# Performance work log

Measured on AMD Instinct MI355X. Metric: run time of the kernel, lower is better.

Reference implementation:

```python
import jax, jax.numpy as jnp
import numpy as np
from jax import lax

EPS = 1e-4  # BatchNorm eps from the module

def maxpool2x2(x):
    # x: [N, C, H, W] -> 2x2 max pool, stride 2, no padding
    return lax.reduce_window(x, -jnp.inf, lax.max, (1, 1, 2, 2), (1, 1, 2, 2), 'VALID')

def conv_nchw(x, w):
    return lax.conv_general_dilated(x, w, window_strides=(1, 1), padding='VALID',
                                    dimension_numbers=('NCHW', 'OIHW', 'NCHW'))

def setup_inputs() -> dict:
    key = jax.random.key(0)
    ks = jax.random.split(key, 6)
    return {
        'x':       jax.random.normal(ks[0], (8192, 1, 32, 32), dtype=jnp.float32),
        'conv1_w': jax.random.normal(ks[1], (20, 1, 5, 5), dtype=jnp.float32) * 0.1,
        'conv2_w': jax.random.normal(ks[2], (50, 20, 5, 5), dtype=jnp.float32) * 0.1,
        'lin_w':   jax.random.normal(ks[3], (500, 1250), dtype=jnp.float32) * 0.05,
        'fc_w':    jax.random.normal(ks[4], (10, 500), dtype=jnp.float32) * 0.05,
        'fc_b':    jax.random.normal(ks[5], (10,), dtype=jnp.float32) * 0.05,
    }

def reference(x, conv1_w, conv2_w, lin_w, fc_w, fc_b):
    # --- features ---
    # Conv2d(1, 20, k=5, bias=False): [N,1,32,32] -> [N,20,28,28]
    h = conv_nchw(x, conv1_w)
    # BatchNorm2d(20, eps=1e-4, affine=False), training-mode batch stats (biased var)
    mean = jnp.mean(h, axis=(0, 2, 3), keepdims=True)
    var = jnp.var(h, axis=(0, 2, 3), keepdims=True)
    h = (h - mean) * lax.rsqrt(var + EPS)
    # ReLU + MaxPool 2x2: -> [N,20,14,14]
    h = maxpool2x2(jnp.maximum(h, 0.0))
    # Binarize(): sign of activations
    h = jnp.sign(h)
    # Conv2dBinary(20, 50, k=5): XNOR-style conv = conv with sign(W), scaled by
    # per-output-channel alpha = mean(|W|). -> [N,50,10,10]
    alpha2 = jnp.mean(jnp.abs(conv2_w), axis=(1, 2, 3)).reshape(1, -1, 1, 1)
    h = conv_nchw(h, jnp.sign(conv2_w)) * alpha2
    # Hardtanh + MaxPool 2x2: -> [N,50,5,5]
    h = maxpool2x2(jnp.clip(h, -1.0, 1.0))
    # --- dense ---
    h = h.reshape(h.shape[0], -1)  # [N, 1250], channel-major like torch.flatten
    h = jnp.sign(h)
    # LinearBinary(1250, 500): y = x @ sign(W)^T * alpha, alpha = mean(|W|, dim=1)
    alpha_l = jnp.mean(jnp.abs(lin_w), axis=1)  # [500]
    h = (h @ jnp.sign(lin_w).T) * alpha_l
    h = jnp.clip(h, -1.0, 1.0)
    # fc: Linear(500, num_classes)
    return h @ fc_w.T + fc_b
```

## Files before the change

kernel.cpp:

```cpp
#include <hip/hip_runtime.h>
#include <stdint.h>


#define NIMG 8192

typedef __attribute__((ext_vector_type(8))) _Float16 f16x8;
typedef __attribute__((ext_vector_type(16))) float f32x16;


__global__ __launch_bounds__(256) void prepsum_k(const float* __restrict__ lw,
                                                 const float* __restrict__ w2,
                                                 const float* __restrict__ x,
                                                 unsigned long long* __restrict__ lwp,
                                                 float* __restrict__ alpha,
                                                 uint32_t* __restrict__ wp2,
                                                 float* __restrict__ partial) {
  int b = blockIdx.x, tid = threadIdx.x;
  if (b < 125) {
    int wave = tid >> 6, lane = tid & 63;
    int j = b * 4 + wave;
    float pa = 0.f;
    for (int k = lane; k < 1250; k += 64) pa += fabsf(lw[j * 1250 + k]);
    for (int o = 32; o > 0; o >>= 1) pa += __shfl_down(pa, o, 64);
    if (lane == 0) alpha[j] = pa / 1250.0f;
    if (lane < 20) {
      unsigned long long m = 0;
      int base = j * 1250 + lane * 64;
      int lim = 1250 - lane * 64; if (lim > 64) lim = 64;
      for (int bb = 0; bb < lim; ++bb)
        if (lw[base + bb] > 0.f) m |= (1ull << bb);
      lwp[j * 20 + lane] = m;
    }
  } else if (b < 130) {
    int idx = (b - 125) * 256 + tid;
    if (idx < 1250) {
      int oc = idx / 25, k = idx % 25;
      uint32_t m = 0;
      for (int ic = 0; ic < 20; ++ic)
        if (w2[(oc * 20 + ic) * 25 + k] > 0.f) m |= (1u << ic);
      wp2[idx] = m;
    }
  } else {
    int sb = b - 130;
    const float4* xv = (const float4*)x + (size_t)sb * 16 * 256;
    float ax = 0.f, ay = 0.f, az = 0.f, aw = 0.f;
    for (int nn = 0; nn < 16; ++nn) {
      float4 v = xv[nn * 256 + tid];
      ax += v.x; ay += v.y; az += v.z; aw += v.w;
    }
    float4 r; r.x = ax; r.y = ay; r.z = az; r.w = aw;
    ((float4*)(partial + (size_t)sb * 1024))[tid] = r;
  }
}

__global__ __launch_bounds__(256) void reduce_k(const float* __restrict__ partial,
                                                float* __restrict__ partial2) {
  int b = blockIdx.x, tid = threadIdx.x;
  int e = (b & 3) * 256 + tid;
  int p0 = (b >> 2) * 32;
  float s = 0.f;
#pragma unroll
  for (int p = 0; p < 32; ++p) s += partial[(size_t)(p0 + p) * 1024 + e];
  partial2[(size_t)(b >> 2) * 1024 + e] = s;
}

__global__ __launch_bounds__(256) void mean_k(const float* __restrict__ partial2,
                                              const float* __restrict__ w1,
                                              float* __restrict__ mean) {
  __shared__ float Tsh[1024];
  __shared__ double U8[25][8];
  __shared__ double U[25];
  int t = threadIdx.x;
  for (int e = t; e < 1024; e += 256) {
    double s = 0.0;
#pragma unroll
    for (int b = 0; b < 16; ++b) s += (double)partial2[b * 1024 + e];
    Tsh[e] = (float)s;
  }
  __syncthreads();
  if (t < 200) {
    int tap = t >> 3, part = t & 7;
    int ky = tap / 5, kx = tap % 5;
    double s = 0.0;
    for (int p = part * 98; p < part * 98 + 98; ++p) {
      int py = p / 28, px = p % 28;
      s += (double)Tsh[(py + ky) * 32 + px + kx];
    }
    U8[tap][part] = s;
  }
  __syncthreads();
  if (t < 25) {
    double s = 0.0;
    for (int i = 0; i < 8; ++i) s += U8[t][i];
    U[t] = s;
  }
  __syncthreads();
  if (t < 20) {
    double s = 0.0;
    for (int q = 0; q < 25; ++q) s += (double)w1[t * 25 + q] * U[q];
    mean[t] = (float)(s / (8192.0 * 784.0));
  }
}

__device__ inline uint32_t pack_f16_pair(float fv) {
  _Float16 h = (_Float16)fv;
  float rem = fv - (float)h;
  _Float16 l = (_Float16)(rem * 4096.0f);
  uint32_t hb = (uint32_t)__builtin_bit_cast(unsigned short, h);
  uint32_t lb = (uint32_t)__builtin_bit_cast(unsigned short, l);
  return (hb << 16) | lb;
}

__global__ __launch_bounds__(256, 6) void conv1_mfma_k(const float* __restrict__ x,
                                                       const float* __restrict__ w1,
                                                       const float* __restrict__ mean,
                                                       uint32_t* __restrict__ b1p) {
  __shared__ uint32_t ximg[2][1032];
  int tid = threadIdx.x;
  int wave = tid >> 6, lane = tid & 63;
  int img = wave >> 1, half = wave & 1;
  int n = blockIdx.x * 2 + img;
  uint32_t* xs = ximg[img];

  const float4* xin = (const float4*)(x + (size_t)n * 1024);
#pragma unroll
  for (int i = 0; i < 2; ++i) {
    int idx = (half * 2 + i) * 64 + lane;
    float4 v = xin[idx];
    float fv[4] = {v.x, v.y, v.z, v.w};
#pragma unroll
    for (int e = 0; e < 4; ++e)
      xs[4 * idx + e] = pack_f16_pair(fv[e]);
  }
  if (half == 0 && lane < 8) xs[1024 + lane] = 0;

  int bc = lane & 31;
  int khsel = lane >> 5;
  f16x8 Bh[2], Bhs[2], Bl[2];
  const int t1tab[8] = {8, 9, 18, 19, 20, 21, 22, 23};
  const _Float16 SC = (_Float16)4096.0f;
#pragma unroll
  for (int j = 0; j < 8; ++j) {
    int t0 = j + khsel * 10;
    float wv0 = (bc < 20) ? w1[bc * 25 + t0] : 0.f;
    uint32_t p0 = pack_f16_pair(wv0);
    _Float16 h0 = __builtin_bit_cast(_Float16, (unsigned short)(p0 >> 16));
    Bh[0][j] = h0;
    Bhs[0][j] = h0 * SC;
    Bl[0][j] = __builtin_bit_cast(_Float16, (unsigned short)(p0 & 0xffffu));
    float wv1 = 0.f;
    if (bc < 20) {
      if (khsel == 0) wv1 = w1[bc * 25 + t1tab[j]];
      else if (j == 4) wv1 = w1[bc * 25 + 24];
    }
    uint32_t p1 = pack_f16_pair(wv1);
    _Float16 h1 = __builtin_bit_cast(_Float16, (unsigned short)(p1 >> 16));
    Bh[1][j] = h1;
    Bhs[1][j] = h1 * SC;
    Bl[1][j] = __builtin_bit_cast(_Float16, (unsigned short)(p1 & 0xffffu));
  }
  float mv = (bc < 20) ? mean[bc] * 4096.0f : 3.0e38f;

  int m = lane & 31;
  int d0 = m + khsel * 64;
  int d1 = m + khsel * 4;

  __syncthreads();

  int pp0 = half * 7;
  for (int pp = pp0; pp < pp0 + 7; ++pp) {
    unsigned long long bacc[16];
#pragma unroll
    for (int r = 0; r < 16; ++r) bacc[r] = 0ull;
#pragma unroll
    for (int py2 = 0; py2 < 2; ++py2) {
      int pybase = (2 * pp + py2) * 32;
      const uint32_t* b0 = xs + pybase + d0;
      const uint32_t* b1 = xs + pybase + d1;
      uint32_t raw[16];
      raw[0] = b0[0];   raw[1] = b0[1];   raw[2] = b0[2];   raw[3] = b0[3];
      raw[4] = b0[4];   raw[5] = b0[32];  raw[6] = b0[33];  raw[7] = b0[34];
      raw[8] = b1[35];  raw[9] = b1[36];  raw[10] = b1[99]; raw[11] = b1[100];
      raw[12] = b1[128]; raw[13] = b1[129]; raw[14] = b1[130]; raw[15] = b1[131];
      f16x8 Ah[2], Al[2];
#pragma unroll
      for (int kh = 0; kh < 2; ++kh) {
        uint32_t hw[4], lw2[4];
#pragma unroll
        for (int jj = 0; jj < 4; ++jj) {
          uint32_t v0 = raw[kh * 8 + 2 * jj], v1 = raw[kh * 8 + 2 * jj + 1];
          hw[jj] = __builtin_amdgcn_perm(v1, v0, 0x07060302u);
          lw2[jj] = __builtin_amdgcn_perm(v1, v0, 0x05040100u);
        }
        struct U4 { uint32_t a, b, c, d; };
        U4 hv4 = {hw[0], hw[1], hw[2], hw[3]};
        U4 lv4 = {lw2[0], lw2[1], lw2[2], lw2[3]};
        Ah[kh] = __builtin_bit_cast(f16x8, hv4);
        Al[kh] = __builtin_bit_cast(f16x8, lv4);
      }
      f32x16 acc;
#pragma unroll
      for (int i = 0; i < 16; ++i) acc[i] = 0.f;
      acc = __builtin_amdgcn_mfma_f32_32x32x16_f16(Ah[0], Bhs[0], acc, 0, 0, 0);
      acc = __builtin_amdgcn_mfma_f32_32x32x16_f16(Ah[1], Bhs[1], acc, 0, 0, 0);
      acc = __builtin_amdgcn_mfma_f32_32x32x16_f16(Ah[0], Bl[0], acc, 0, 0, 0);
      acc = __builtin_amdgcn_mfma_f32_32x32x16_f16(Ah[1], Bl[1], acc, 0, 0, 0);
      acc = __builtin_amdgcn_mfma_f32_32x32x16_f16(Al[0], Bh[0], acc, 0, 0, 0);
      acc = __builtin_amdgcn_mfma_f32_32x32x16_f16(Al[1], Bh[1], acc, 0, 0, 0);
#pragma unroll
      for (int r = 0; r < 16; ++r)
        bacc[r] |= __ballot(acc[r] > mv);
    }
    uint32_t pm = 0;
#pragma unroll
    for (int pc = 0; pc < 14; ++pc) {
      int px0 = 2 * pc;
      int r0 = (px0 & 3) + 4 * (px0 >> 3);
      int h0 = (px0 >> 2) & 1;
      unsigned long long mm = bacc[r0] | bacc[r0 + 1];
      uint32_t val = (uint32_t)(mm >> (32 * h0));
      if (lane == pc) pm = val;
    }
    if (lane < 14) b1p[(size_t)n * 196 + pp * 14 + lane] = pm;
  }
}

__global__ __launch_bounds__(512) void conv2lin_k(const uint32_t* __restrict__ b1p,
                                                  const uint32_t* __restrict__ wp2,
                                                  const unsigned long long* __restrict__ lwp,
                                                  const float* __restrict__ alpha,
                                                  const float* __restrict__ fcw,
                                                  const float* __restrict__ fcb,
                                                  float* __restrict__ out) {
  __shared__ uint32_t wsh[1250];
  __shared__ uint32_t bm[8][196];
  __shared__ int sumpc[8][100];
  __shared__ char uni[8][2048];
  int tid = threadIdx.x;
  int wave = tid >> 6, lane = tid & 63;
  int n = blockIdx.x * 8 + wave;
  signed char* s2w = (signed char*)uni[wave];
  float* hshw = (float*)uni[wave];

  for (int i = tid; i < 1250; i += 512) wsh[i] = wp2[i];
#pragma unroll
  for (int rd = 0; rd < 4; ++rd) {
    int idx = rd * 64 + lane;
    if (idx < 196) bm[wave][idx] = b1p[(size_t)n * 196 + idx];
  }
  __syncthreads();

#pragma unroll
  for (int rd = 0; rd < 2; ++rd) {
    int pp = rd * 64 + lane;
    if (pp < 100) {
      int Y = pp / 10, X = pp % 10, s = 0;
#pragma unroll
      for (int ky = 0; ky < 5; ++ky)
#pragma unroll
        for (int kx = 0; kx < 5; ++kx)
          s += __popc(bm[wave][(Y + ky) * 14 + X + kx]);
      sumpc[wave][pp] = s;
    }
  }

#pragma unroll
  for (int rd = 0; rd < 4; ++rd) {
    int unit = rd * 64 + lane;
    if (unit < 250) {
      int oc = unit / 5, r = unit % 5;
      uint32_t w[25];
#pragma unroll
      for (int i = 0; i < 25; ++i) w[i] = wsh[oc * 25 + i];
      for (int pc = 0; pc < 5; ++pc) {
        uint32_t pa[6][6];
#pragma unroll
        for (int rr = 0; rr < 6; ++rr)
#pragma unroll
          for (int cc = 0; cc < 6; ++cc)
            pa[rr][cc] = bm[wave][(2 * r + rr) * 14 + 2 * pc + cc];
        int best = -1000000;
#pragma unroll
        for (int dy = 0; dy < 2; ++dy)
#pragma unroll
          for (int dx = 0; dx < 2; ++dx) {
            int a = 0;
#pragma unroll
            for (int ky = 0; ky < 5; ++ky)
#pragma unroll
              for (int kx = 0; kx < 5; ++kx)
                a += __popc(w[ky * 5 + kx] & pa[dy + ky][dx + kx]);
            a = 2 * a - sumpc[wave][(2 * r + dy) * 10 + 2 * pc + dx];
            if (a > best) best = a;
          }
        s2w[5 * unit + pc] = (signed char)((best > 0) - (best < 0));
      }
    }
  }
  if (lane < 30) s2w[1250 + lane] = 0;

  unsigned long long Pm[20], Nm[20];
  int cp = 0, cn = 0;
#pragma unroll
  for (int k = 0; k < 20; ++k) {
    signed char v = s2w[k * 64 + lane];
    unsigned long long P = __ballot(v > 0);
    unsigned long long N = __ballot(v < 0);
    Pm[k] = P; Nm[k] = N;
    cp += __popcll(P); cn += __popcll(N);
  }

#pragma unroll
  for (int rd = 0; rd < 8; ++rd) {
    int j = rd * 64 + lane;
    float y = 0.f;
    if (j < 500) {
      const ulonglong2* W2 = (const ulonglong2*)(lwp + (size_t)j * 20);
      int a = 0, b = 0;
#pragma unroll
      for (int i = 0; i < 10; ++i) {
        ulonglong2 w2v = W2[i];
        a += __popcll(w2v.x & Pm[2 * i]) + __popcll(w2v.y & Pm[2 * i + 1]);
        b += __popcll(w2v.x & Nm[2 * i]) + __popcll(w2v.y & Nm[2 * i + 1]);
      }
      int dot = 2 * (a - b) - cp + cn;
      y = alpha[j] * (float)dot;
      y = fminf(1.0f, fmaxf(-1.0f, y));
    }
    hshw[rd * 64 + lane] = y;
  }

  float hv[8];
#pragma unroll
  for (int k = 0; k < 8; ++k) hv[k] = hshw[k * 64 + lane];
#pragma unroll
  for (int o = 0; o < 10; ++o) {
    float pa = 0.f;
#pragma unroll
    for (int k = 0; k < 8; ++k) {
      int j = k * 64 + lane;
      if (j < 500) pa += hv[k] * fcw[o * 500 + j];
    }
    for (int off = 32; off > 0; off >>= 1) pa += __shfl_down(pa, off, 64);
    if (lane == 0) out[(size_t)n * 10 + o] = pa + fcb[o];
  }
}

extern "C" void kernel_launch(void* const* d_in, const int* in_sizes, int n_in,
                              void* d_out, int out_size, void* d_ws, size_t ws_size,
                              hipStream_t stream) {
  const float* x   = (const float*)d_in[0];
  const float* w1  = (const float*)d_in[1];
  const float* w2  = (const float*)d_in[2];
  const float* lw  = (const float*)d_in[3];
  const float* fcw = (const float*)d_in[4];
  const float* fcb = (const float*)d_in[5];
  float* out = (float*)d_out;
  char* ws = (char*)d_ws;

  float*    mean  = (float*)(ws + 0);
  uint32_t* wp2   = (uint32_t*)(ws + 128);
  float*    alpha = (float*)(ws + 5632);
  unsigned long long* lwp = (unsigned long long*)(ws + 7680);
  float*    partial = (float*)(ws + 87808);
  uint32_t* b1p   = (uint32_t*)(ws + 2184960);
  float*    partial2 = (float*)(ws + 8607488);

  prepsum_k<<<642, 256, 0, stream>>>(lw, w2, x, lwp, alpha, wp2, partial);
  reduce_k<<<64, 256, 0, stream>>>(partial, partial2);
  mean_k<<<1, 256, 0, stream>>>(partial2, w1, mean);
  conv1_mfma_k<<<4096, 256, 0, stream>>>(x, w1, mean, b1p);
  conv2lin_k<<<1024, 512, 0, stream>>>(b1p, wp2, lwp, alpha, fcw, fcb, out);
}
```

Baseline: 236.9 us.

## Replace popcount binary conv2 with int8 MFMA on unpacked sign planes

The binary conv2 used to run as per-lane AND/popcount loops over packed channel masks. It now runs as int8 32x32x32 MFMA. Activations are expanded in shared memory into 0/1 byte planes per pixel, and weights are pre-packed into ±1 int8 fragments in the prep kernel. The output rows are arranged so that each group of four accumulator entries maps to one 2x2 pool window, which lets the max-pool and sign be applied directly from registers. The cost is a larger shared-memory footprint (about 50KB for planes) and extra prep blocks, and it assumes the MFMA register layouts are correct.

```diff
diff --git a/kernel.cpp b/kernel.cpp
--- a/kernel.cpp
+++ b/kernel.cpp
@@ -6,6 +6,8 @@
 
 typedef __attribute__((ext_vector_type(8))) _Float16 f16x8;
 typedef __attribute__((ext_vector_type(16))) float f32x16;
+typedef __attribute__((ext_vector_type(4))) int i32x4;
+typedef __attribute__((ext_vector_type(16))) int i32x16;
 
 
 __global__ __launch_bounds__(256) void prepsum_k(const float* __restrict__ lw,
@@ -13,7 +15,7 @@
                                                  const float* __restrict__ x,
                                                  unsigned long long* __restrict__ lwp,
                                                  float* __restrict__ alpha,
-                                                 uint32_t* __restrict__ wp2,
+                                                 i32x4* __restrict__ bg,
                                                  float* __restrict__ partial) {
   int b = blockIdx.x, tid = threadIdx.x;
   if (b < 125) {
@@ -31,17 +33,33 @@
         if (lw[base + bb] > 0.f) m |= (1ull << bb);
       lwp[j * 20 + lane] = m;
     }
-  } else if (b < 130) {
+  } else if (b < 138) {
     int idx = (b - 125) * 256 + tid;
-    if (idx < 1250) {
-      int oc = idx / 25, k = idx % 25;
-      uint32_t m = 0;
-      for (int ic = 0; ic < 20; ++ic)
-        if (w2[(oc * 20 + ic) * 25 + k] > 0.f) m |= (1u << ic);
-      wp2[idx] = m;
+    if (idx < 3200) {
+      int t = idx >> 7;
+      int rem = idx & 127;
+      int l = rem & 63;
+      int nt = rem >> 6;
+      int oc = nt * 32 + (l & 31);
+      int hi = l >> 5;
+      i32x4 o4;
+#pragma unroll
+      for (int wi = 0; wi < 4; ++wi) {
+        int word = 0;
+#pragma unroll
+        for (int bb = 0; bb < 4; ++bb) {
+          int k = hi * 16 + wi * 4 + bb;
+          int v = 0;
+          if (k < 20 && oc < 50)
+            v = (w2[(oc * 20 + k) * 25 + t] > 0.f) ? 1 : -1;
+          word |= (v & 0xff) << (8 * bb);
+        }
+        o4[wi] = word;
+      }
+      bg[idx] = o4;
     }
   } else {
-    int sb = b - 130;
+    int sb = b - 138;
     const float4* xv = (const float4*)x + (size_t)sb * 16 * 256;
     float ax = 0.f, ay = 0.f, az = 0.f, aw = 0.f;
     for (int nn = 0; nn < 16; ++nn) {
@@ -225,78 +243,91 @@
   }
 }
 
-__global__ __launch_bounds__(512) void conv2lin_k(const uint32_t* __restrict__ b1p,
-                                                  const uint32_t* __restrict__ wp2,
-                                                  const unsigned long long* __restrict__ lwp,
-                                                  const float* __restrict__ alpha,
-                                                  const float* __restrict__ fcw,
-                                                  const float* __restrict__ fcb,
-                                                  float* __restrict__ out) {
-  __shared__ uint32_t wsh[1250];
-  __shared__ uint32_t bm[8][196];
-  __shared__ int sumpc[8][100];
-  __shared__ char uni[8][2048];
+__global__ __launch_bounds__(512, 4) void conv2lin_k(const uint32_t* __restrict__ b1p,
+                                                     const i32x4* __restrict__ bg,
+                                                     const unsigned long long* __restrict__ lwp,
+                                                     const float* __restrict__ alpha,
+                                                     const float* __restrict__ fcw,
+                                                     const float* __restrict__ fcb,
+                                                     float* __restrict__ out) {
+  __shared__ __attribute__((aligned(16))) char planes[8 * 196 * 32];
+  __shared__ __attribute__((aligned(16))) char uni[8][2048];
   int tid = threadIdx.x;
   int wave = tid >> 6, lane = tid & 63;
-  int n = blockIdx.x * 8 + wave;
+  int n0 = blockIdx.x * 8;
+
+#pragma unroll
+  for (int r = 0; r < 4; ++r) {
+    int idx = r * 512 + tid;
+    if (idx < 1568) {
+      uint32_t w = b1p[(size_t)n0 * 196 + idx];
+      i32x4 lo, hi4;
+#pragma unroll
+      for (int j = 0; j < 4; ++j)
+        lo[j] = (int)((((w >> (4 * j)) & 0xFu) * 0x00204081u) & 0x01010101u);
+#pragma unroll
+      for (int j = 0; j < 4; ++j)
+        hi4[j] = (int)((((w >> (4 * j + 16)) & 0xFu) * 0x00204081u) & 0x01010101u);
+      *(i32x4*)(planes + idx * 32) = lo;
+      *(i32x4*)(planes + idx * 32 + 16) = hi4;
+    }
+  }
+  __syncthreads();
+
+  {
+    int m = lane & 31, hi = lane >> 5;
+    for (int mt = wave; mt < 25; mt += 8) {
+      int qg = mt * 8 + (m >> 2);
+      int img = (qg * 41) >> 10;
+      int quad = qg - img * 25;
+      int Y = (quad * 13) >> 6;
+      int X = quad - Y * 5;
+      int px = (2 * Y + ((m >> 1) & 1)) * 14 + 2 * X + (m & 1);
+      const char* ab = planes + ((img * 196 + px) * 32 + hi * 16);
+      const i32x4* bgl = bg + lane;
+      i32x16 acc0, acc1;
+#pragma unroll
+      for (int i = 0; i < 16; ++i) { acc0[i] = 0; acc1[i] = 0; }
+#pragma unroll 1
+      for (int ky = 0; ky < 5; ++ky) {
+        const char* ab2 = ab + ky * 14 * 32;
+        const i32x4* bg2 = bgl + ky * 5 * 128;
+#pragma unroll
+        for (int kx = 0; kx < 5; ++kx) {
+          i32x4 av = *(const i32x4*)(ab2 + kx * 32);
+          i32x4 bv0 = bg2[kx * 128];
+          i32x4 bv1 = bg2[kx * 128 + 64];
+          acc0 = __builtin_amdgcn_mfma_i32_32x32x32_i8(av, bv0, acc0, 0, 0, 0);
+          acc1 = __builtin_amdgcn_mfma_i32_32x32x32_i8(av, bv1, acc1, 0, 0, 0);
+        }
+      }
+      int oc0 = m, oc1 = 32 + m;
+#pragma unroll
+      for (int g = 0; g < 4; ++g) {
+        int qloc = 2 * g + hi;
+        int qg2 = mt * 8 + qloc;
+        int img2 = (qg2 * 41) >> 10;
+        int quad2 = qg2 - img2 * 25;
+        {
+          int a0 = acc0[4 * g], a1 = acc0[4 * g + 1], a2 = acc0[4 * g + 2], a3 = acc0[4 * g + 3];
+          int c0 = a0 > a1 ? a0 : a1, c1 = a2 > a3 ? a2 : a3;
+          int best = c0 > c1 ? c0 : c1;
+          uni[img2][oc0 * 25 + quad2] = (char)((best > 0) - (best < 0));
+        }
+        if (oc1 < 50) {
+          int a0 = acc1[4 * g], a1 = acc1[4 * g + 1], a2 = acc1[4 * g + 2], a3 = acc1[4 * g + 3];
+          int c0 = a0 > a1 ? a0 : a1, c1 = a2 > a3 ? a2 : a3;
+          int best = c0 > c1 ? c0 : c1;
+          uni[img2][oc1 * 25 + quad2] = (char)((best > 0) - (best < 0));
+        }
+      }
+    }
+  }
+  __syncthreads();
+
+  int n = n0 + wave;
   signed char* s2w = (signed char*)uni[wave];
   float* hshw = (float*)uni[wave];
-
-  for (int i = tid; i < 1250; i += 512) wsh[i] = wp2[i];
-#pragma unroll
-  for (int rd = 0; rd < 4; ++rd) {
-    int idx = rd * 64 + lane;
-    if (idx < 196) bm[wave][idx] = b1p[(size_t)n * 196 + idx];
-  }
-  __syncthreads();
-
-#pragma unroll
-  for (int rd = 0; rd < 2; ++rd) {
-    int pp = rd * 64 + lane;
-    if (pp < 100) {
-      int Y = pp / 10, X = pp % 10, s = 0;
-#pragma unroll
-      for (int ky = 0; ky < 5; ++ky)
-#pragma unroll
-        for (int kx = 0; kx < 5; ++kx)
-          s += __popc(bm[wave][(Y + ky) * 14 + X + kx]);
-      sumpc[wave][pp] = s;
-    }
-  }
-
-#pragma unroll
-  for (int rd = 0; rd < 4; ++rd) {
-    int unit = rd * 64 + lane;
-    if (unit < 250) {
-      int oc = unit / 5, r = unit % 5;
-      uint32_t w[25];
-#pragma unroll
-      for (int i = 0; i < 25; ++i) w[i] = wsh[oc * 25 + i];
-      for (int pc = 0; pc < 5; ++pc) {
-        uint32_t pa[6][6];
-#pragma unroll
-        for (int rr = 0; rr < 6; ++rr)
-#pragma unroll
-          for (int cc = 0; cc < 6; ++cc)
-            pa[rr][cc] = bm[wave][(2 * r + rr) * 14 + 2 * pc + cc];
-        int best = -1000000;
-#pragma unroll
-        for (int dy = 0; dy < 2; ++dy)
-#pragma unroll
-          for (int dx = 0; dx < 2; ++dx) {
-            int a = 0;
-#pragma unroll
-            for (int ky = 0; ky < 5; ++ky)
-#pragma unroll
-              for (int kx = 0; kx < 5; ++kx)
-                a += __popc(w[ky * 5 + kx] & pa[dy + ky][dx + kx]);
-            a = 2 * a - sumpc[wave][(2 * r + dy) * 10 + 2 * pc + dx];
-            if (a > best) best = a;
-          }
-        s2w[5 * unit + pc] = (signed char)((best > 0) - (best < 0));
-      }
-    }
-  }
   if (lane < 30) s2w[1250 + lane] = 0;
 
   unsigned long long Pm[20], Nm[20];
@@ -359,16 +390,16 @@
   char* ws = (char*)d_ws;
 
   float*    mean  = (float*)(ws + 0);
-  uint32_t* wp2   = (uint32_t*)(ws + 128);
   float*    alpha = (float*)(ws + 5632);
   unsigned long long* lwp = (unsigned long long*)(ws + 7680);
   float*    partial = (float*)(ws + 87808);
   uint32_t* b1p   = (uint32_t*)(ws + 2184960);
   float*    partial2 = (float*)(ws + 8607488);
-
-  prepsum_k<<<642, 256, 0, stream>>>(lw, w2, x, lwp, alpha, wp2, partial);
+  i32x4*    bg    = (i32x4*)(ws + 8673024);
+
+  prepsum_k<<<650, 256, 0, stream>>>(lw, w2, x, lwp, alpha, bg, partial);
   reduce_k<<<64, 256, 0, stream>>>(partial, partial2);
   mean_k<<<1, 256, 0, stream>>>(partial2, w1, mean);
   conv1_mfma_k<<<4096, 256, 0, stream>>>(x, w1, mean, b1p);
-  conv2lin_k<<<1024, 512, 0, stream>>>(b1p, wp2, lwp, alpha, fcw, fcb, out);
-}
+  conv2lin_k<<<1024, 512, 0, stream>>>(b1p, bg, lwp, alpha, fcw, fcb, out);
+}
```

New measurement: 229.4 us. 1.03x faster.
